# Kernel optimization log

Measured on AMD Instinct MI355X. Metric: run time of the kernel, lower is better.

The kernel has to match this reference:

```python
import jax, jax.numpy as jnp
import numpy as np

N, F, D = 32, 1024, 512
H = 2 * D  # dim * ratio
EPS = 1e-5


def batchnorm1d(x, gamma, beta):
    # x: (N, F, L); BatchNorm1d over channel dim F, stats over (N, L) (training mode, biased var)
    mean = jnp.mean(x, axis=(0, 2), keepdims=True)
    var = jnp.var(x, axis=(0, 2), keepdims=True)
    xn = (x - mean) * jax.lax.rsqrt(var + EPS)
    return xn * gamma[None, :, None] + beta[None, :, None]


def setup_inputs() -> dict:
    key = jax.random.key(0)
    ks = jax.random.split(key, 5)
    x = jax.random.normal(ks[0], (N, F, D), dtype=jnp.float32)
    W0 = jax.random.normal(ks[1], (H, D), dtype=jnp.float32) * 0.02  # Linear(D->H) weight (out,in)
    b0 = jnp.zeros((H,), jnp.float32)
    W1 = jax.random.normal(ks[2], (D, H), dtype=jnp.float32) * 0.02  # Linear(H->D)
    b1 = jnp.zeros((D,), jnp.float32)
    Wc = jax.random.normal(ks[3], (F, F), dtype=jnp.float32) * 0.02  # Conv1d k=1 weight (out_ch,in_ch)
    bc = jnp.zeros((F,), jnp.float32)
    ones = jnp.ones((F,), jnp.float32)
    zeros = jnp.zeros((F,), jnp.float32)
    return {
        "x": x,
        "W0": W0, "b0": b0, "g0": ones, "be0": zeros,
        "W1": W1, "b1": b1, "g1": ones, "be1": zeros,
        "gf": ones, "bf": zeros,
        "Wc": Wc, "bc": bc,
        "go": ones, "bo": zeros,
    }


def reference(x, W0, b0, g0, be0, W1, b1, g1, be1, gf, bf, Wc, bc, go, bo):
    # proj_mlp0: Linear(D->H) + BN1d(F)
    v = jnp.einsum('nfd,hd->nfh', x, W0) + b0  # (N, F, H)
    v = batchnorm1d(v, g0, be0)
    # correlation: bmm(v, v^T) -> softsign -> bmm(w, v)
    w = jnp.einsum('nfh,ngh->nfg', v, v)  # (N, F, F)
    w = w / (1.0 + jnp.abs(w))  # softsign
    v = jnp.einsum('nfg,ngh->nfh', w, v)  # (N, F, H)
    # proj_mlp1: Linear(H->D) + BN1d(F)
    v = jnp.einsum('nfh,dh->nfd', v, W1) + b1  # (N, F, D)
    v = batchnorm1d(v, g1, be1)
    # feed_norm(v + x)
    xr = batchnorm1d(v + x, gf, bf)
    # proj_conv: Conv1d(F->F, kernel=1) over channel dim
    v = jnp.einsum('oi,nid->nod', Wc, xr) + bc[None, :, None]
    return batchnorm1d(v + xr, go, bo)
```

## Files before the change

### kernel.cpp

```cpp
#include <hip/hip_runtime.h>
#include <stdint.h>

#define NB 32
#define FC 1024
#define DD 512
#define HH 1024
#define BN_EPS 1e-5f

typedef unsigned short u16;
typedef unsigned int u32;
typedef __attribute__((ext_vector_type(8))) short bf16x8;
typedef __attribute__((ext_vector_type(4))) float f32x4;
typedef __attribute__((ext_vector_type(8))) unsigned short ushort8v;

#define AS1 __attribute__((address_space(1)))
#define AS3 __attribute__((address_space(3)))

__device__ __forceinline__ float b2f(u16 u) {
    union { u32 i; float f; } v;
    v.i = ((u32)u) << 16;
    return v.f;
}
__device__ __forceinline__ u16 f2b(float f) {
    union { float f; u32 i; } v;
    v.f = f;
    const u32 b = v.i;
    return (u16)((b + 0x7FFFu + ((b >> 16) & 1u)) >> 16);
}

__device__ __forceinline__ void gld16(const u16* g, u16* l) {
    __builtin_amdgcn_global_load_lds((const AS1 u32*)g, (AS3 u32*)l, 16, 0, 0);
}

__device__ __forceinline__ void swizzle_tiles(int& mt, int& nt, int& zt) {
    const int gx = gridDim.x, gy = gridDim.y, gz = gridDim.z;
    const int mzTot = gy * gz;
    if ((mzTot & 7) != 0) { nt = blockIdx.x; mt = blockIdx.y; zt = blockIdx.z; return; }
    long lin = ((long)blockIdx.z * gy + blockIdx.y) * gx + blockIdx.x;
    const int slab = mzTot >> 3;
    const int xcd = (int)(lin & 7);
    const long idx = lin >> 3;
    nt = (int)(idx % gx);
    const int mz = (int)(idx / gx) + xcd * slab;
    mt = mz % gy;
    zt = mz / gy;
}

__global__ __launch_bounds__(256) void detect_dtype(
    const u32* __restrict__ x, int* __restrict__ flag)
{
    __shared__ int cnt[256];
    int c = 0;
    for (int i = threadIdx.x; i < 4096; i += 256) {
        const u32 lo = x[i] & 0xFFFFu;
        const u32 e = (lo >> 7) & 0xFFu;
        if (e >= 0x68u && e <= 0x85u) c++;
    }
    cnt[threadIdx.x] = c;
    __syncthreads();
    for (int s = 128; s > 0; s >>= 1) {
        if (threadIdx.x < (unsigned)s) cnt[threadIdx.x] += cnt[threadIdx.x + s];
        __syncthreads();
    }
    if (threadIdx.x == 0) flag[0] = (cnt[0] > 2048) ? 1 : 0;
}

__global__ __launch_bounds__(256) void convert_to_bf16(
    const void* __restrict__ src, u16* __restrict__ dst, long n4,
    const int* __restrict__ flag)
{
    const bool isbf = (*flag != 0);
    long i4 = (long)blockIdx.x * blockDim.x + threadIdx.x;
    const long stride = (long)gridDim.x * blockDim.x;
    for (; i4 < n4; i4 += stride) {
        const long i = i4 << 2;
        if (isbf) {
            *(ushort4*)(dst + i) = *(const ushort4*)((const u16*)src + i);
        } else {
            const float4 v = *(const float4*)((const float*)src + i);
            ushort4 o;
            o.x = f2b(v.x); o.y = f2b(v.y); o.z = f2b(v.z); o.w = f2b(v.w);
            *(ushort4*)(dst + i) = o;
        }
    }
}

template<bool BIAS, bool SOFTSIGN>
__global__ __launch_bounds__(512, 2) void gemm256_nt(
    const u16* __restrict__ A, const u16* __restrict__ B,
    const u16* __restrict__ bias, u16* __restrict__ C,
    int M, int N, int K, int lda, int ldb, int ldc,
    long sA, long sB, long sC)
{
    extern __shared__ char smem[];

    int mt, nt, zt;
    swizzle_tiles(mt, nt, zt);
    const u16* Ab = A + (long)zt * sA + (long)(mt * 256) * lda;
    const u16* Bb = B + (long)zt * sB + (long)(nt * 256) * ldb;
    C += (long)zt * sC;

    const int tid  = threadIdx.x;
    const int lane = tid & 63;
    const int wv   = tid >> 6;
    const int wr   = (wv >> 2) * 128;
    const int wc   = (wv & 3) * 64;
    const int lm   = lane & 15;
    const int q    = lane >> 4;

    int aOff[2][4], bOff[2][2];
    #pragma unroll
    for (int mh = 0; mh < 2; ++mh)
        #pragma unroll
        for (int i = 0; i < 4; ++i) {
            const int r = wr + mh * 64 + i * 16 + lm;
            aOff[mh][i] = r * 64 + ((q ^ ((r >> 1) & 3)) << 4);
        }
    #pragma unroll
    for (int nh = 0; nh < 2; ++nh)
        #pragma unroll
        for (int j = 0; j < 2; ++j) {
            const int r = wc + nh * 32 + j * 16 + lm;
            bOff[nh][j] = r * 64 + ((q ^ ((r >> 1) & 3)) << 4);
        }

    const int rw = lane >> 2, qs = lane & 3;
    const u16* pA[2]; const u16* pB[2];
    int ldsC[2];
    #pragma unroll
    for (int c = 0; c < 2; ++c) {
        const int r = wv * 32 + c * 16 + rw;
        const int kq = (qs ^ ((r >> 1) & 3)) << 3;
        pA[c] = Ab + (long)r * lda + kq;
        pB[c] = Bb + (long)r * ldb + kq;
        ldsC[c] = wv * 2048 + c * 1024;
    }

#define STG(bufOff, op, kh, c, PX, kofs) \
    gld16((PX)[c] + (kofs) + (kh) * 32, \
          (u16*)(smem + (bufOff) + (op) * 32768 + (kh) * 16384 + ldsC[c]))

#define RDA(mh, kk, bo) { \
    const char* base_ = smem + (bo) + (kk) * 16384; \
    a[0] = *(const bf16x8*)(base_ + aOff[mh][0]); \
    a[1] = *(const bf16x8*)(base_ + aOff[mh][1]); \
    a[2] = *(const bf16x8*)(base_ + aOff[mh][2]); \
    a[3] = *(const bf16x8*)(base_ + aOff[mh][3]); }

#define RDB(nh, kk, bo) { \
    const char* base_ = smem + (bo) + 32768 + (kk) * 16384; \
    b[0] = *(const bf16x8*)(base_ + bOff[nh][0]); \
    b[1] = *(const bf16x8*)(base_ + bOff[nh][1]); }

#define MMA(mh, nh) do { \
    __builtin_amdgcn_s_setprio(1); \
    acc[(mh)*4+0][(nh)*2+0] = __builtin_amdgcn_mfma_f32_16x16x32_bf16(a[0], b[0], acc[(mh)*4+0][(nh)*2+0], 0,0,0); \
    acc[(mh)*4+0][(nh)*2+1] = __builtin_amdgcn_mfma_f32_16x16x32_bf16(a[0], b[1], acc[(mh)*4+0][(nh)*2+1], 0,0,0); \
    acc[(mh)*4+1][(nh)*2+0] = __builtin_amdgcn_mfma_f32_16x16x32_bf16(a[1], b[0], acc[(mh)*4+1][(nh)*2+0], 0,0,0); \
    acc[(mh)*4+1][(nh)*2+1] = __builtin_amdgcn_mfma_f32_16x16x32_bf16(a[1], b[1], acc[(mh)*4+1][(nh)*2+1], 0,0,0); \
    acc[(mh)*4+2][(nh)*2+0] = __builtin_amdgcn_mfma_f32_16x16x32_bf16(a[2], b[0], acc[(mh)*4+2][(nh)*2+0], 0,0,0); \
    acc[(mh)*4+2][(nh)*2+1] = __builtin_amdgcn_mfma_f32_16x16x32_bf16(a[2], b[1], acc[(mh)*4+2][(nh)*2+1], 0,0,0); \
    acc[(mh)*4+3][(nh)*2+0] = __builtin_amdgcn_mfma_f32_16x16x32_bf16(a[3], b[0], acc[(mh)*4+3][(nh)*2+0], 0,0,0); \
    acc[(mh)*4+3][(nh)*2+1] = __builtin_amdgcn_mfma_f32_16x16x32_bf16(a[3], b[1], acc[(mh)*4+3][(nh)*2+1], 0,0,0); \
    __builtin_amdgcn_s_setprio(0); \
} while (0)

#define BAR() __builtin_amdgcn_s_barrier()
#define WAIT_VM4() { asm volatile("s_waitcnt vmcnt(4)" ::: "memory"); \
                     __builtin_amdgcn_sched_barrier(0); }

    f32x4 acc[8][4] = {};
    bf16x8 a[4], b[2];

    const int NT = K >> 6;

    STG(0, 0, 0, 0, pA, 0); STG(0, 0, 0, 1, pA, 0);
    STG(0, 1, 0, 0, pB, 0); STG(0, 1, 0, 1, pB, 0);
    STG(0, 0, 1, 0, pA, 0); STG(0, 0, 1, 1, pA, 0);
    STG(0, 1, 1, 0, pB, 0); STG(0, 1, 1, 1, pB, 0);
    WAIT_VM4();
    BAR();

    for (int t = 0; t < NT; ++t) {
        const int bo = (t & 1) * 65536;
        const int bn = ((t + 1) & 1) * 65536;
        const int kn = ((t + 1 < NT) ? (t + 1) : t) * 64;

        RDA(0, 0, bo); RDB(0, 0, bo);
        STG(bn, 0, 0, 0, pA, kn);
        BAR(); MMA(0, 0); BAR();
        RDB(1, 0, bo);
        STG(bn, 0, 0, 1, pA, kn);
        BAR(); MMA(0, 1); BAR();
        RDA(1, 0, bo);
        STG(bn, 1, 0, 0, pB, kn);
        BAR(); MMA(1, 1); BAR();
        RDB(0, 0, bo);
        STG(bn, 1, 0, 1, pB, kn);
        WAIT_VM4();
        BAR(); MMA(1, 0); BAR();
        RDA(0, 1, bo); RDB(0, 1, bo);
        STG(bn, 0, 1, 0, pA, kn);
        BAR(); MMA(0, 0); BAR();
        RDB(1, 1, bo);
        STG(bn, 0, 1, 1, pA, kn);
        BAR(); MMA(0, 1); BAR();
        RDA(1, 1, bo);
        STG(bn, 1, 1, 0, pB, kn);
        BAR(); MMA(1, 1); BAR();
        RDB(0, 1, bo);
        STG(bn, 1, 1, 1, pB, kn);
        WAIT_VM4();
        BAR(); MMA(1, 0); BAR();
    }

#undef STG
#undef RDA
#undef RDB
#undef MMA
#undef BAR
#undef WAIT_VM4

    __syncthreads();
    float* rep = (float*)smem + wv * (16 * 65);
    const int rr = lane >> 2;
    const int cg = lane & 3;
    const int m0 = mt * 256;
    const int n0 = nt * 256;
    #pragma unroll
    for (int i = 0; i < 8; ++i) {
        #pragma unroll
        for (int j = 0; j < 4; ++j) {
            const int col = 16 * j + lm;
            const float bj = BIAS ? b2f(bias[n0 + wc + col]) : 0.0f;
            #pragma unroll
            for (int r = 0; r < 4; ++r) {
                float v = acc[i][j][r] + bj;
                if (SOFTSIGN) v = v / (1.0f + fabsf(v));
                rep[(q * 4 + r) * 65 + col] = v;
            }
        }
        const float* lr = rep + rr * 65 + cg * 16;
        const float4 f0 = *(const float4*)(lr + 0);
        const float4 f1 = *(const float4*)(lr + 4);
        const float4 f2 = *(const float4*)(lr + 8);
        const float4 f3 = *(const float4*)(lr + 12);
        ushort8v o0, o1;
        o0[0] = f2b(f0.x); o0[1] = f2b(f0.y); o0[2] = f2b(f0.z); o0[3] = f2b(f0.w);
        o0[4] = f2b(f1.x); o0[5] = f2b(f1.y); o0[6] = f2b(f1.z); o0[7] = f2b(f1.w);
        o1[0] = f2b(f2.x); o1[1] = f2b(f2.y); o1[2] = f2b(f2.z); o1[3] = f2b(f2.w);
        o1[4] = f2b(f3.x); o1[5] = f2b(f3.y); o1[6] = f2b(f3.z); o1[7] = f2b(f3.w);
        u16* cp = C + (long)(m0 + wr + 16 * i + rr) * ldc + n0 + wc + cg * 16;
        *(ushort8v*)cp = o0;
        *(ushort8v*)(cp + 8) = o1;
    }
}

__global__ __launch_bounds__(256) void transpose_bf16(
    const u16* __restrict__ src, u16* __restrict__ dst,
    int R, int Cc, long sS, long sD)
{
    __shared__ u16 t[32][33];
    const int bz = blockIdx.z;
    src += (long)bz * sS;
    dst += (long)bz * sD;
    const int c0 = blockIdx.x * 32;
    const int r0 = blockIdx.y * 32;
    const int lx = threadIdx.x & 31;
    const int ly = threadIdx.x >> 5;
    #pragma unroll
    for (int d = 0; d < 32; d += 8)
        t[ly + d][lx] = src[(long)(r0 + ly + d) * Cc + c0 + lx];
    __syncthreads();
    #pragma unroll
    for (int d = 0; d < 32; d += 8)
        dst[(long)(c0 + ly + d) * R + r0 + lx] = t[lx][ly + d];
}

__global__ __launch_bounds__(256) void bn_stats(
    const u16* __restrict__ src, const u16* __restrict__ gamma,
    const u16* __restrict__ beta, float* __restrict__ ss,
    int Lc, int nOuter)
{
    const int f = blockIdx.x;
    const long outerStride = (long)FC * Lc;
    const u16* base = src + (long)f * Lc;

    float s1 = 0.f, s2 = 0.f;
    for (int n = 0; n < nOuter; ++n) {
        const u16* p = base + n * outerStride;
        for (int i = (threadIdx.x << 2); i < Lc; i += (blockDim.x << 2)) {
            const ushort4 v = *(const ushort4*)(p + i);
            const float a = b2f(v.x), b = b2f(v.y), c = b2f(v.z), d = b2f(v.w);
            s1 += a + b + c + d;
            s2 += a * a + b * b + c * c + d * d;
        }
    }

    __shared__ float r1[256], r2[256];
    const int tid = threadIdx.x;
    r1[tid] = s1;
    r2[tid] = s2;
    __syncthreads();
    for (int s = 128; s > 0; s >>= 1) {
        if (tid < s) { r1[tid] += r1[tid + s]; r2[tid] += r2[tid + s]; }
        __syncthreads();
    }
    if (tid == 0) {
        const float cnt  = (float)nOuter * (float)Lc;
        const float mean = r1[0] / cnt;
        const float var  = r2[0] / cnt - mean * mean;
        const float rstd = rsqrtf(var + BN_EPS);
        const float sc   = b2f(gamma[f]) * rstd;
        ss[f]      = sc;
        ss[FC + f] = b2f(beta[f]) - mean * sc;
    }
}

template<bool ADD>
__global__ __launch_bounds__(256) void bn_apply(
    const u16* __restrict__ src, const void* __restrict__ add,
    const int* __restrict__ addflag,
    const float* __restrict__ ss, void* __restrict__ dst,
    const int* __restrict__ outflag, long total4, int Lc)
{
    const bool addf32 = ADD && (addflag != nullptr) && (*addflag == 0);
    const bool outf32 = (outflag != nullptr) && (*outflag == 0);
    long i4 = (long)blockIdx.x * blockDim.x + threadIdx.x;
    const long stride = (long)gridDim.x * blockDim.x;
    for (; i4 < total4; i4 += stride) {
        const long i = i4 << 2;
        const int c = (int)((i / Lc) % FC);
        const float sc = ss[c];
        const float sh = ss[FC + c];
        const ushort4 v = *(const ushort4*)(src + i);
        float o0 = fmaf(b2f(v.x), sc, sh);
        float o1 = fmaf(b2f(v.y), sc, sh);
        float o2 = fmaf(b2f(v.z), sc, sh);
        float o3 = fmaf(b2f(v.w), sc, sh);
        if (ADD) {
            if (addf32) {
                const float4 a = *(const float4*)((const float*)add + i);
                o0 += a.x; o1 += a.y; o2 += a.z; o3 += a.w;
            } else {
                const ushort4 a = *(const ushort4*)((const u16*)add + i);
                o0 += b2f(a.x); o1 += b2f(a.y); o2 += b2f(a.z); o3 += b2f(a.w);
            }
        }
        if (outf32) {
            float4 o; o.x = o0; o.y = o1; o.z = o2; o.w = o3;
            *(float4*)((float*)dst + i) = o;
        } else {
            ushort4 o;
            o.x = f2b(o0); o.y = f2b(o1); o.z = f2b(o2); o.w = f2b(o3);
            *(ushort4*)((u16*)dst + i) = o;
        }
    }
}

__global__ __launch_bounds__(256) void add3_bias(
    const u16* __restrict__ a, const u16* __restrict__ b,
    const u16* __restrict__ bias, u16* __restrict__ dst,
    long total4, int Lc)
{
    long i4 = (long)blockIdx.x * blockDim.x + threadIdx.x;
    const long stride = (long)gridDim.x * blockDim.x;
    for (; i4 < total4; i4 += stride) {
        const long i = i4 << 2;
        const int c = (int)((i / Lc) % FC);
        const float bs = b2f(bias[c]);
        const ushort4 va = *(const ushort4*)(a + i);
        const ushort4 vb = *(const ushort4*)(b + i);
        ushort4 o;
        o.x = f2b(b2f(va.x) + b2f(vb.x) + bs);
        o.y = f2b(b2f(va.y) + b2f(vb.y) + bs);
        o.z = f2b(b2f(va.z) + b2f(vb.z) + bs);
        o.w = f2b(b2f(va.w) + b2f(vb.w) + bs);
        *(ushort4*)(dst + i) = o;
    }
}

extern "C" void kernel_launch(void* const* d_in, const int* in_sizes, int n_in,
                              void* d_out, int out_size, void* d_ws, size_t ws_size,
                              hipStream_t stream)
{
    const size_t MiB = (size_t)1 << 20;
    const long sFH = (long)FC * HH;
    const long sFF = (long)FC * FC;
    const long sFD = (long)FC * DD;
    const long VE  = (long)NB * FC * HH;
    const long PE  = (long)NB * FC * DD;

    const size_t GLDS = 131072;
    static bool s_attr = false;
    if (!s_attr) {
        s_attr = true;
        hipFuncSetAttribute(reinterpret_cast<const void*>(&gemm256_nt<true, false>),
                            hipFuncAttributeMaxDynamicSharedMemorySize, (int)GLDS);
        hipFuncSetAttribute(reinterpret_cast<const void*>(&gemm256_nt<false, true>),
                            hipFuncAttributeMaxDynamicSharedMemorySize, (int)GLDS);
        hipFuncSetAttribute(reinterpret_cast<const void*>(&gemm256_nt<false, false>),
                            hipFuncAttributeMaxDynamicSharedMemorySize, (int)GLDS);
    }

    long off[16];
    long cur = 0;
    for (int i = 1; i < 15; ++i) { off[i] = cur; cur += ((long)in_sizes[i] + 7) & ~7L; }
    const size_t paramBytes = (size_t)cur * 2;

    int cb = 16;
    while (cb > 1 &&
           64 * MiB + (size_t)cb * 6 * MiB + paramBytes + 16384 > ws_size)
        cb >>= 1;

    u16* V   = (u16*)d_ws;
    u16* VT  = (u16*)((char*)d_ws + 64 * MiB);
    u16* WW  = VT + (long)cb * sFH;
    u16* V2  = WW + (long)cb * sFF;
    u16* WC  = V2 + (long)cb * sFH;
    char* tail = (char*)(WC + cur);
    tail = (char*)(((uintptr_t)tail + 255) & ~(uintptr_t)255);
    float* SS   = (float*)tail;
    int*   FLAG = (int*)(SS + 2 * FC);
    u16* VX  = (u16*)d_out;
    u16* XB  = (u16*)d_out + PE;
    u16* V4  = V;
    u16* XRT = V + PE;

    const dim3 blk(256);
    const dim3 blk512(512);
    const dim3 egrid(4096);

    detect_dtype<<<1, blk, 0, stream>>>((const u32*)d_in[0], FLAG);
    for (int i = 1; i < 15; ++i) {
        const long n4 = (long)in_sizes[i] / 4;
        int g = (int)((n4 + 255) / 256);
        if (g > 1024) g = 1024;
        if (g < 1) g = 1;
        convert_to_bf16<<<dim3(g), blk, 0, stream>>>(d_in[i], WC + off[i], n4, FLAG);
    }
    convert_to_bf16<<<dim3(1024), blk, 0, stream>>>(d_in[0], XB, PE / 4, FLAG);

    const u16* W0c = WC + off[1];
    const u16* b0c = WC + off[2];
    const u16* g0c = WC + off[3];
    const u16* be0c = WC + off[4];
    const u16* W1c = WC + off[5];
    const u16* b1c = WC + off[6];
    const u16* g1c = WC + off[7];
    const u16* be1c = WC + off[8];
    const u16* gfc = WC + off[9];
    const u16* bfc = WC + off[10];
    const u16* Wcc = WC + off[11];
    const u16* bcc = WC + off[12];
    const u16* goc = WC + off[13];
    const u16* boc = WC + off[14];

    gemm256_nt<true, false><<<dim3(HH / 256, (NB * FC) / 256, 1), blk512, GLDS, stream>>>(
        XB, W0c, b0c, V, NB * FC, HH, DD, DD, DD, HH, 0, 0, 0);

    bn_stats<<<FC, blk, 0, stream>>>(V, g0c, be0c, SS, HH, NB);
    bn_apply<false><<<egrid, blk, 0, stream>>>(V, nullptr, nullptr, SS, V, nullptr, VE / 4, HH);

    for (int bz0 = 0; bz0 < NB; bz0 += cb) {
        const int c = (NB - bz0 < cb) ? (NB - bz0) : cb;
        transpose_bf16<<<dim3(HH / 32, FC / 32, c), blk, 0, stream>>>(
            V + bz0 * sFH, VT, FC, HH, sFH, sFH);
        gemm256_nt<false, true><<<dim3(FC / 256, FC / 256, c), blk512, GLDS, stream>>>(
            V + bz0 * sFH, V + bz0 * sFH, nullptr, WW,
            FC, FC, HH, HH, HH, FC, sFH, sFH, sFF);
        gemm256_nt<false, false><<<dim3(HH / 256, FC / 256, c), blk512, GLDS, stream>>>(
            WW, VT, nullptr, V2,
            FC, HH, FC, FC, FC, HH, sFF, sFH, sFH);
        gemm256_nt<true, false><<<dim3(DD / 256, (c * FC) / 256, 1), blk512, GLDS, stream>>>(
            V2, W1c, b1c, VX + bz0 * sFD,
            c * FC, DD, HH, HH, HH, DD, 0, 0, 0);
    }

    bn_stats<<<FC, blk, 0, stream>>>(VX, g1c, be1c, SS, DD, NB);
    bn_apply<true><<<egrid, blk, 0, stream>>>(VX, XB, nullptr, SS, VX, nullptr, PE / 4, DD);

    bn_stats<<<FC, blk, 0, stream>>>(VX, gfc, bfc, SS, DD, NB);
    bn_apply<false><<<egrid, blk, 0, stream>>>(VX, nullptr, nullptr, SS, VX, nullptr, PE / 4, DD);

    transpose_bf16<<<dim3(DD / 32, FC / 32, NB), blk, 0, stream>>>(
        VX, XRT, FC, DD, sFD, sFD);
    gemm256_nt<false, false><<<dim3(DD / 256, FC / 256, NB), blk512, GLDS, stream>>>(
        Wcc, XRT, nullptr, V4, FC, DD, FC, FC, FC, DD, 0, sFD, sFD);

    add3_bias<<<egrid, blk, 0, stream>>>(V4, VX, bcc, V4, PE / 4, DD);

    bn_stats<<<FC, blk, 0, stream>>>(V4, goc, boc, SS, DD, NB);
    bn_apply<false><<<egrid, blk, 0, stream>>>(V4, nullptr, nullptr, SS, d_out, FLAG, PE / 4, DD);
}
```

Measured before the change: 712.3 us.

## Use 4-stage K=32 GEMM pipeline, parallelize bn_stats loads, shift-based channel index

New measurement: 690.3 us. -3.1%, faster.

```diff
diff --git a/kernel.cpp b/kernel.cpp
--- a/kernel.cpp
+++ b/kernel.cpp
@@ -108,7 +108,7 @@
     const int lm   = lane & 15;
     const int q    = lane >> 4;
 
-    int aOff[2][4], bOff[2][2];
+    int aOff[2][4], bOff[4];
     #pragma unroll
     for (int mh = 0; mh < 2; ++mh)
         #pragma unroll
@@ -117,12 +117,10 @@
             aOff[mh][i] = r * 64 + ((q ^ ((r >> 1) & 3)) << 4);
         }
     #pragma unroll
-    for (int nh = 0; nh < 2; ++nh)
-        #pragma unroll
-        for (int j = 0; j < 2; ++j) {
-            const int r = wc + nh * 32 + j * 16 + lm;
-            bOff[nh][j] = r * 64 + ((q ^ ((r >> 1) & 3)) << 4);
-        }
+    for (int j = 0; j < 4; ++j) {
+        const int r = wc + j * 16 + lm;
+        bOff[j] = r * 64 + ((q ^ ((r >> 1) & 3)) << 4);
+    }
 
     const int rw = lane >> 2, qs = lane & 3;
     const u16* pA[2]; const u16* pB[2];
@@ -136,92 +134,86 @@
         ldsC[c] = wv * 2048 + c * 1024;
     }
 
-#define STG(bufOff, op, kh, c, PX, kofs) \
-    gld16((PX)[c] + (kofs) + (kh) * 32, \
-          (u16*)(smem + (bufOff) + (op) * 32768 + (kh) * 16384 + ldsC[c]))
-
-#define RDA(mh, kk, bo) { \
-    const char* base_ = smem + (bo) + (kk) * 16384; \
+#define STAGE(bufOff, kofs) { \
+    gld16(pA[0] + (kofs), (u16*)(smem + (bufOff) + ldsC[0])); \
+    gld16(pA[1] + (kofs), (u16*)(smem + (bufOff) + ldsC[1])); \
+    gld16(pB[0] + (kofs), (u16*)(smem + (bufOff) + 16384 + ldsC[0])); \
+    gld16(pB[1] + (kofs), (u16*)(smem + (bufOff) + 16384 + ldsC[1])); }
+
+#define RDA(mh, bo) { \
+    const char* base_ = smem + (bo); \
     a[0] = *(const bf16x8*)(base_ + aOff[mh][0]); \
     a[1] = *(const bf16x8*)(base_ + aOff[mh][1]); \
     a[2] = *(const bf16x8*)(base_ + aOff[mh][2]); \
     a[3] = *(const bf16x8*)(base_ + aOff[mh][3]); }
 
-#define RDB(nh, kk, bo) { \
-    const char* base_ = smem + (bo) + 32768 + (kk) * 16384; \
-    b[0] = *(const bf16x8*)(base_ + bOff[nh][0]); \
-    b[1] = *(const bf16x8*)(base_ + bOff[nh][1]); }
-
-#define MMA(mh, nh) do { \
+#define RDB(bo) { \
+    const char* base_ = smem + (bo) + 16384; \
+    b[0] = *(const bf16x8*)(base_ + bOff[0]); \
+    b[1] = *(const bf16x8*)(base_ + bOff[1]); \
+    b[2] = *(const bf16x8*)(base_ + bOff[2]); \
+    b[3] = *(const bf16x8*)(base_ + bOff[3]); }
+
+#define MMA(mh) do { \
     __builtin_amdgcn_s_setprio(1); \
-    acc[(mh)*4+0][(nh)*2+0] = __builtin_amdgcn_mfma_f32_16x16x32_bf16(a[0], b[0], acc[(mh)*4+0][(nh)*2+0], 0,0,0); \
-    acc[(mh)*4+0][(nh)*2+1] = __builtin_amdgcn_mfma_f32_16x16x32_bf16(a[0], b[1], acc[(mh)*4+0][(nh)*2+1], 0,0,0); \
-    acc[(mh)*4+1][(nh)*2+0] = __builtin_amdgcn_mfma_f32_16x16x32_bf16(a[1], b[0], acc[(mh)*4+1][(nh)*2+0], 0,0,0); \
-    acc[(mh)*4+1][(nh)*2+1] = __builtin_amdgcn_mfma_f32_16x16x32_bf16(a[1], b[1], acc[(mh)*4+1][(nh)*2+1], 0,0,0); \
-    acc[(mh)*4+2][(nh)*2+0] = __builtin_amdgcn_mfma_f32_16x16x32_bf16(a[2], b[0], acc[(mh)*4+2][(nh)*2+0], 0,0,0); \
-    acc[(mh)*4+2][(nh)*2+1] = __builtin_amdgcn_mfma_f32_16x16x32_bf16(a[2], b[1], acc[(mh)*4+2][(nh)*2+1], 0,0,0); \
-    acc[(mh)*4+3][(nh)*2+0] = __builtin_amdgcn_mfma_f32_16x16x32_bf16(a[3], b[0], acc[(mh)*4+3][(nh)*2+0], 0,0,0); \
-    acc[(mh)*4+3][(nh)*2+1] = __builtin_amdgcn_mfma_f32_16x16x32_bf16(a[3], b[1], acc[(mh)*4+3][(nh)*2+1], 0,0,0); \
+    acc[(mh)*4+0][0] = __builtin_amdgcn_mfma_f32_16x16x32_bf16(a[0], b[0], acc[(mh)*4+0][0], 0,0,0); \
+    acc[(mh)*4+0][1] = __builtin_amdgcn_mfma_f32_16x16x32_bf16(a[0], b[1], acc[(mh)*4+0][1], 0,0,0); \
+    acc[(mh)*4+0][2] = __builtin_amdgcn_mfma_f32_16x16x32_bf16(a[0], b[2], acc[(mh)*4+0][2], 0,0,0); \
+    acc[(mh)*4+0][3] = __builtin_amdgcn_mfma_f32_16x16x32_bf16(a[0], b[3], acc[(mh)*4+0][3], 0,0,0); \
+    acc[(mh)*4+1][0] = __builtin_amdgcn_mfma_f32_16x16x32_bf16(a[1], b[0], acc[(mh)*4+1][0], 0,0,0); \
+    acc[(mh)*4+1][1] = __builtin_amdgcn_mfma_f32_16x16x32_bf16(a[1], b[1], acc[(mh)*4+1][1], 0,0,0); \
+    acc[(mh)*4+1][2] = __builtin_amdgcn_mfma_f32_16x16x32_bf16(a[1], b[2], acc[(mh)*4+1][2], 0,0,0); \
+    acc[(mh)*4+1][3] = __builtin_amdgcn_mfma_f32_16x16x32_bf16(a[1], b[3], acc[(mh)*4+1][3], 0,0,0); \
+    acc[(mh)*4+2][0] = __builtin_amdgcn_mfma_f32_16x16x32_bf16(a[2], b[0], acc[(mh)*4+2][0], 0,0,0); \
+    acc[(mh)*4+2][1] = __builtin_amdgcn_mfma_f32_16x16x32_bf16(a[2], b[1], acc[(mh)*4+2][1], 0,0,0); \
+    acc[(mh)*4+2][2] = __builtin_amdgcn_mfma_f32_16x16x32_bf16(a[2], b[2], acc[(mh)*4+2][2], 0,0,0); \
+    acc[(mh)*4+2][3] = __builtin_amdgcn_mfma_f32_16x16x32_bf16(a[2], b[3], acc[(mh)*4+2][3], 0,0,0); \
+    acc[(mh)*4+3][0] = __builtin_amdgcn_mfma_f32_16x16x32_bf16(a[3], b[0], acc[(mh)*4+3][0], 0,0,0); \
+    acc[(mh)*4+3][1] = __builtin_amdgcn_mfma_f32_16x16x32_bf16(a[3], b[1], acc[(mh)*4+3][1], 0,0,0); \
+    acc[(mh)*4+3][2] = __builtin_amdgcn_mfma_f32_16x16x32_bf16(a[3], b[2], acc[(mh)*4+3][2], 0,0,0); \
+    acc[(mh)*4+3][3] = __builtin_amdgcn_mfma_f32_16x16x32_bf16(a[3], b[3], acc[(mh)*4+3][3], 0,0,0); \
     __builtin_amdgcn_s_setprio(0); \
 } while (0)
 
 #define BAR() __builtin_amdgcn_s_barrier()
-#define WAIT_VM4() { asm volatile("s_waitcnt vmcnt(4)" ::: "memory"); \
+#define WAIT_VM8() { asm volatile("s_waitcnt vmcnt(8)" ::: "memory"); \
                      __builtin_amdgcn_sched_barrier(0); }
 
     f32x4 acc[8][4] = {};
-    bf16x8 a[4], b[2];
-
-    const int NT = K >> 6;
-
-    STG(0, 0, 0, 0, pA, 0); STG(0, 0, 0, 1, pA, 0);
-    STG(0, 1, 0, 0, pB, 0); STG(0, 1, 0, 1, pB, 0);
-    STG(0, 0, 1, 0, pA, 0); STG(0, 0, 1, 1, pA, 0);
-    STG(0, 1, 1, 0, pB, 0); STG(0, 1, 1, 1, pB, 0);
-    WAIT_VM4();
+    bf16x8 a[4], b[4];
+
+    const int NT = K >> 5;
+
+    STAGE(0, 0);
+    STAGE(32768, 32);
+    STAGE(65536, 64);
+    WAIT_VM8();
     BAR();
 
     for (int t = 0; t < NT; ++t) {
-        const int bo = (t & 1) * 65536;
-        const int bn = ((t + 1) & 1) * 65536;
-        const int kn = ((t + 1 < NT) ? (t + 1) : t) * 64;
-
-        RDA(0, 0, bo); RDB(0, 0, bo);
-        STG(bn, 0, 0, 0, pA, kn);
-        BAR(); MMA(0, 0); BAR();
-        RDB(1, 0, bo);
-        STG(bn, 0, 0, 1, pA, kn);
-        BAR(); MMA(0, 1); BAR();
-        RDA(1, 0, bo);
-        STG(bn, 1, 0, 0, pB, kn);
-        BAR(); MMA(1, 1); BAR();
-        RDB(0, 0, bo);
-        STG(bn, 1, 0, 1, pB, kn);
-        WAIT_VM4();
-        BAR(); MMA(1, 0); BAR();
-        RDA(0, 1, bo); RDB(0, 1, bo);
-        STG(bn, 0, 1, 0, pA, kn);
-        BAR(); MMA(0, 0); BAR();
-        RDB(1, 1, bo);
-        STG(bn, 0, 1, 1, pA, kn);
-        BAR(); MMA(0, 1); BAR();
-        RDA(1, 1, bo);
-        STG(bn, 1, 1, 0, pB, kn);
-        BAR(); MMA(1, 1); BAR();
-        RDB(0, 1, bo);
-        STG(bn, 1, 1, 1, pB, kn);
-        WAIT_VM4();
-        BAR(); MMA(1, 0); BAR();
-    }
-
-#undef STG
+        const int bo = (t & 3) * 32768;
+        const int bn = ((t + 3) & 3) * 32768;
+        const int kn = ((t + 3 < NT) ? (t + 3) : (NT - 1)) * 32;
+
+        RDA(0, bo); RDB(bo);
+        STAGE(bn, kn);
+        BAR(); MMA(0); BAR();
+        RDA(1, bo);
+        WAIT_VM8();
+        BAR(); MMA(1); BAR();
+    }
+
+#undef STAGE
 #undef RDA
 #undef RDB
 #undef MMA
 #undef BAR
-#undef WAIT_VM4
-
+#undef WAIT_VM8
+
+    asm volatile("s_waitcnt vmcnt(0)" ::: "memory");
+    __builtin_amdgcn_sched_barrier(0);
     __syncthreads();
+
     float* rep = (float*)smem + wv * (16 * 65);
     const int rr = lane >> 2;
     const int cg = lane & 3;
@@ -286,10 +278,16 @@
     const long outerStride = (long)FC * Lc;
     const u16* base = src + (long)f * Lc;
 
+    const int vecs = Lc >> 2;
+    const int tpn  = (vecs < 256) ? vecs : 256;
+    const int nGrp = 256 / tpn;
+    const int sub  = threadIdx.x / tpn;
+    const int off4 = (threadIdx.x % tpn) << 2;
+
     float s1 = 0.f, s2 = 0.f;
-    for (int n = 0; n < nOuter; ++n) {
-        const u16* p = base + n * outerStride;
-        for (int i = (threadIdx.x << 2); i < Lc; i += (blockDim.x << 2)) {
+    for (int n = sub; n < nOuter; n += nGrp) {
+        const u16* p = base + (long)n * outerStride;
+        for (int i = off4; i < Lc; i += (tpn << 2)) {
             const ushort4 v = *(const ushort4*)(p + i);
             const float a = b2f(v.x), b = b2f(v.y), c = b2f(v.z), d = b2f(v.w);
             s1 += a + b + c + d;
@@ -322,7 +320,7 @@
     const u16* __restrict__ src, const void* __restrict__ add,
     const int* __restrict__ addflag,
     const float* __restrict__ ss, void* __restrict__ dst,
-    const int* __restrict__ outflag, long total4, int Lc)
+    const int* __restrict__ outflag, long total4, int lcShift)
 {
     const bool addf32 = ADD && (addflag != nullptr) && (*addflag == 0);
     const bool outf32 = (outflag != nullptr) && (*outflag == 0);
@@ -330,7 +328,7 @@
     const long stride = (long)gridDim.x * blockDim.x;
     for (; i4 < total4; i4 += stride) {
         const long i = i4 << 2;
-        const int c = (int)((i / Lc) % FC);
+        const int c = (int)((i >> lcShift) & (FC - 1));
         const float sc = ss[c];
         const float sh = ss[FC + c];
         const ushort4 v = *(const ushort4*)(src + i);
@@ -361,13 +359,13 @@
 __global__ __launch_bounds__(256) void add3_bias(
     const u16* __restrict__ a, const u16* __restrict__ b,
     const u16* __restrict__ bias, u16* __restrict__ dst,
-    long total4, int Lc)
+    long total4, int lcShift)
 {
     long i4 = (long)blockIdx.x * blockDim.x + threadIdx.x;
     const long stride = (long)gridDim.x * blockDim.x;
     for (; i4 < total4; i4 += stride) {
         const long i = i4 << 2;
-        const int c = (int)((i / Lc) % FC);
+        const int c = (int)((i >> lcShift) & (FC - 1));
         const float bs = b2f(bias[c]);
         const ushort4 va = *(const ushort4*)(a + i);
         const ushort4 vb = *(const ushort4*)(b + i);
@@ -460,7 +458,7 @@
         XB, W0c, b0c, V, NB * FC, HH, DD, DD, DD, HH, 0, 0, 0);
 
     bn_stats<<<FC, blk, 0, stream>>>(V, g0c, be0c, SS, HH, NB);
-    bn_apply<false><<<egrid, blk, 0, stream>>>(V, nullptr, nullptr, SS, V, nullptr, VE / 4, HH);
+    bn_apply<false><<<egrid, blk, 0, stream>>>(V, nullptr, nullptr, SS, V, nullptr, VE / 4, 10);
 
     for (int bz0 = 0; bz0 < NB; bz0 += cb) {
         const int c = (NB - bz0 < cb) ? (NB - bz0) : cb;
@@ -478,18 +476,18 @@
     }
 
     bn_stats<<<FC, blk, 0, stream>>>(VX, g1c, be1c, SS, DD, NB);
-    bn_apply<true><<<egrid, blk, 0, stream>>>(VX, XB, nullptr, SS, VX, nullptr, PE / 4, DD);
+    bn_apply<true><<<egrid, blk, 0, stream>>>(VX, XB, nullptr, SS, VX, nullptr, PE / 4, 9);
 
     bn_stats<<<FC, blk, 0, stream>>>(VX, gfc, bfc, SS, DD, NB);
-    bn_apply<false><<<egrid, blk, 0, stream>>>(VX, nullptr, nullptr, SS, VX, nullptr, PE / 4, DD);
+    bn_apply<false><<<egrid, blk, 0, stream>>>(VX, nullptr, nullptr, SS, VX, nullptr, PE / 4, 9);
 
     transpose_bf16<<<dim3(DD / 32, FC / 32, NB), blk, 0, stream>>>(
         VX, XRT, FC, DD, sFD, sFD);
     gemm256_nt<false, false><<<dim3(DD / 256, FC / 256, NB), blk512, GLDS, stream>>>(
         Wcc, XRT, nullptr, V4, FC, DD, FC, FC, FC, DD, 0, sFD, sFD);
 
-    add3_bias<<<egrid, blk, 0, stream>>>(V4, VX, bcc, V4, PE / 4, DD);
+    add3_bias<<<egrid, blk, 0, stream>>>(V4, VX, bcc, V4, PE / 4, 9);
 
     bn_stats<<<FC, blk, 0, stream>>>(V4, goc, boc, SS, DD, NB);
-    bn_apply<false><<<egrid, blk, 0, stream>>>(V4, nullptr, nullptr, SS, d_out, FLAG, PE / 4, DD);
-}
+    bn_apply<false><<<egrid, blk, 0, stream>>>(V4, nullptr, nullptr, SS, d_out, FLAG, PE / 4, 9);
+}
```
